# Kernel tuning notes

Hardware: AMD Instinct MI355X
Metric: run time of the kernel (lower is better)

## Reference

```python
import jax, jax.numpy as jnp
import numpy as np
from jax import lax


def setup_inputs() -> dict:
    key = jax.random.key(0)
    ks = jax.random.split(key, 9)
    B = 4096
    x = jax.random.normal(ks[0], (B, 1, 28, 28), jnp.float32)

    def init(k, shape, fan_in):
        return (jax.random.normal(k, shape, jnp.float32) / np.float32(np.sqrt(fan_in)))

    W1 = init(ks[1], (32, 1, 3, 3), 1 * 9)
    b1 = init(ks[2], (32,), 1 * 9)
    W2 = init(ks[3], (64, 32, 3, 3), 32 * 9)
    b2 = init(ks[4], (64,), 32 * 9)
    Wl1 = init(ks[5], (14 * 14 * 64, 128), 14 * 14 * 64)
    bl1 = init(ks[6], (128,), 14 * 14 * 64)
    Wl2 = init(ks[7], (128, 10), 128)
    bl2 = init(ks[8], (10,), 128)
    return {"x": x, "W1": W1, "b1": b1, "W2": W2, "b2": b2,
            "Wl1": Wl1, "bl1": bl1, "Wl2": Wl2, "bl2": bl2}


def _conv_same(h, W, b):
    # submanifold sparse conv == SAME-padded dense conv, output restricted to active sites
    y = lax.conv_general_dilated(h, W, window_strides=(1, 1), padding="SAME",
                                 dimension_numbers=("NCHW", "OIHW", "NCHW"))
    return y + b[None, :, None, None]


def reference(x, W1, b1, W2, b2, Wl1, bl1, Wl2, bl2):
    # active-site mask from Voxels.from_dense (nonzero pixels); submanifold convs keep it fixed
    mask = (jnp.abs(x) > 0).any(axis=1, keepdims=True).astype(x.dtype)  # [B,1,28,28]
    h = jax.nn.relu(_conv_same(x, W1, b1) * mask)   # [B,32,28,28]
    h = jax.nn.relu(_conv_same(h, W2, b2) * mask)   # [B,64,28,28]
    # sparse 2x2/2 max pool; inactive sites are 0 and post-ReLU actives are >=0,
    # so dense window max == sparse max, and all-inactive windows densify to 0
    B = h.shape[0]
    h = h.reshape(B, 64, 14, 2, 14, 2).max(axis=(3, 5))  # [B,64,14,14]
    h = h.reshape(B, 64 * 14 * 14)
    # dropout is identity in eval
    h = jax.nn.relu(h @ Wl1 + bl1)
    logits = h @ Wl2 + bl2
    return jax.nn.log_softmax(logits, axis=1)
```

## Files before the change

kernel.cpp:

```cpp
#include <hip/hip_runtime.h>
#include <math.h>

typedef __bf16 bf16;
typedef __bf16 bf16x8 __attribute__((ext_vector_type(8)));
typedef unsigned short u16;
typedef unsigned short u16x4 __attribute__((ext_vector_type(4)));
typedef unsigned short u16x8 __attribute__((ext_vector_type(8)));
typedef float f32x4 __attribute__((ext_vector_type(4)));
typedef float f32x16 __attribute__((ext_vector_type(16)));
typedef unsigned int u32x4 __attribute__((ext_vector_type(4)));

__global__ void prep_all(const float* __restrict__ W2, bf16* __restrict__ w2r,
                         const float* __restrict__ W1, bf16* __restrict__ w1f,
                         const float* __restrict__ Wl1, bf16* __restrict__ wl1t) {
    __shared__ float tile[32 * 129];
    const int b = blockIdx.x;
    const int t = threadIdx.x;
    if (b < 392) {
        const int s  = b >> 1;
        const int cg = b & 1;
        for (int e = t; e < 4096; e += 256) {
            int cl = e >> 7, n = e & 127;
            tile[cl * 129 + n] = Wl1[((long)(cg * 32 + cl) * 196 + s) * 128 + n];
        }
        __syncthreads();
        for (int e = t; e < 4096; e += 256) {
            int n = e >> 5, cl = e & 31;
            wl1t[(long)n * 12544 + s * 64 + cg * 32 + cl] = (bf16)tile[cl * 129 + n];
        }
    } else {
        int e = (b - 392) * 256 + t;
        if (e < 18432) {
            int j  = e & 7;
            int l  = (e >> 3) & 63;
            int f  = e >> 9;
            int s  = f >> 1;
            int nt = f & 1;
            int tap  = s >> 1;
            int ci   = (s & 1) * 16 + (l >> 5) * 8 + j;
            int cout = nt * 32 + (l & 31);
            w2r[e] = (bf16)W2[cout * 288 + ci * 9 + tap];
        } else {
            int e2 = e - 18432;
            if (e2 < 512) {
                int j = e2 & 7;
                int l = e2 >> 3;
                int k = (l >> 5) * 8 + j;
                int n = l & 31;
                w1f[e2] = (k < 9) ? (bf16)W1[n * 9 + k] : (bf16)0.f;
            }
        }
    }
}

__global__ __launch_bounds__(256, 3)
void conv_fused(const float* __restrict__ x, const float* __restrict__ b1,
                const bf16* __restrict__ w2r, const bf16* __restrict__ w1f,
                const float* __restrict__ b2, bf16* __restrict__ pooled)
{
    __shared__ __attribute__((aligned(16))) bf16  h1s[16 * 1032];
    __shared__ __attribute__((aligned(16))) bf16  Aim[512 * 16];
    __shared__ __attribute__((aligned(16))) u16   mrow[512];
    __shared__ __attribute__((aligned(16))) float mneg[98 * 4];
    __shared__ __attribute__((aligned(16))) bf16  xs[640];

    const int t    = threadIdx.x;
    const int lane = t & 63;
    const int wv   = t >> 6;
    const int img  = blockIdx.x >> 1;
    const int hb   = blockIdx.x & 1;
    const int nt   = wv & 1;
    const int wp   = wv >> 1;
    const int ml31 = lane & 31;
    const int lg   = lane >> 5;

    const float* xi = x + img * 784;

    bf16x8 breg[18];
    {
        const bf16x8* wp2 = (const bf16x8*)w2r;
        #pragma unroll
        for (int s = 0; s < 18; s++)
            breg[s] = wp2[(2 * s + nt) * 64 + lane];
    }
    const bf16x8 w1frag = *(const bf16x8*)&w1f[lane * 8];
    const float  b1r    = b1[ml31];
    const float  bias2  = b2[nt * 32 + ml31];

    for (int e = t; e < 640; e += 256) {
        int j  = e >> 5;
        int c  = e & 31;
        int xr = hb * 14 - 2 + j;
        int xc = c - 1;
        float v = 0.f;
        if (xr >= 0 && xr < 28 && xc >= 0 && xc < 28) v = xi[xr * 28 + xc];
        xs[e] = (bf16)v;
    }
    __syncthreads();

    const u16* xu = (const u16*)xs;
    #pragma unroll
    for (int pp = 0; pp < 2; pp++) {
        int p = t + pp * 256;
        int r = p >> 5, c = p & 31;
        int b = r * 32 + c - 1;
        u16 v0 = xu[b],      v1 = xu[b + 1],  v2 = xu[b + 2];
        u16 v3 = xu[b + 32], v4 = xu[b + 33], v5 = xu[b + 34];
        u16 v6 = xu[b + 64], v7 = xu[b + 65], v8 = xu[b + 66];
        u16x8 t0;
        t0[0] = v0; t0[1] = v1; t0[2] = v2; t0[3] = v3;
        t0[4] = v4; t0[5] = v5; t0[6] = v6; t0[7] = v7;
        u16x8 t1;
        #pragma unroll
        for (int j = 0; j < 8; j++) t1[j] = 0;
        t1[0] = v8;
        *(u16x8*)&Aim[p * 16]     = *(u16x8*)&t0;
        *(u16x8*)&Aim[p * 16 + 8] = *(u16x8*)&t1;
        mrow[p] = (c >= 1 && c <= 28 && (v4 & 0x7fff) != 0) ? 1 : 0;
    }
    for (int e = t; e < 392; e += 256) {
        int s   = e >> 2, q = e & 3;
        int spi = s / 14, spj = s - spi * 14;
        u16 cv = xu[(2 * spi + (q >> 1) + 2) * 32 + 2 * spj + (q & 1) + 1];
        mneg[e] = ((cv & 0x7fff) != 0) ? 0.f : -1e30f;
    }
    __syncthreads();

    for (int Mt = wv; Mt < 16; Mt += 4) {
        int m = Mt * 32 + ml31;
        bf16x8 af = *(const bf16x8*)&Aim[m * 16 + lg * 8];
        f32x16 acc;
        #pragma unroll
        for (int e = 0; e < 16; e++) acc[e] = b1r;
        acc = __builtin_amdgcn_mfma_f32_32x32x16_bf16(af, w1frag, acc, 0, 0, 0);
        const int rowb = Mt * 1032;
        #pragma unroll
        for (int run = 0; run < 4; run++) {
            int p0 = Mt * 32 + run * 8 + 4 * lg;
            u16x4 mk = *(const u16x4*)&mrow[p0];
            #pragma unroll
            for (int j = 0; j < 4; j++) {
                float s = acc[run * 4 + j];
                float o = (mk[j] != 0) ? fmaxf(s, 0.f) : 0.f;
                int col = run * 8 + 4 * lg + j;
                int swz = (col & 6) << 2;
                h1s[rowb + col * 32 + (ml31 ^ swz)] = (bf16)o;
            }
        }
    }
    __syncthreads();

    const int half = lg;
    const int cib  = half * 8;

    int q  = ml31 & 3;
    int pj = wp * 8 + (ml31 >> 2);
    int pi = 0;
    if (pj >= 14) { pj -= 14; pi = 1; }

    bf16* pout = pooled + (long)img * 12544 + hb * 98 * 64 + nt * 32 + ml31;

    for (int Mt = wp; Mt < 13; Mt += 2) {
        int row = 2 * pi + (q >> 1);
        if (row > 13) row = 13;
        int colb = 2 * pj + (q & 1);
        int rowb = row * 1032;

        int e0a[3], e1a[3];
        #pragma unroll
        for (int dc = 0; dc < 3; dc++) {
            int cc   = colb + dc;
            int swz  = (cc & 6) << 2;
            int base = rowb + cc * 32;
            e0a[dc] = base + (cib ^ swz);
            e1a[dc] = base + ((16 + cib) ^ swz);
        }

        f32x16 accA, accB = {};
        #pragma unroll
        for (int e = 0; e < 16; e++) accA[e] = bias2;

        #pragma unroll
        for (int dr = 0; dr < 3; dr++) {
            #pragma unroll
            for (int dc = 0; dc < 3; dc++) {
                const int tap = dr * 3 + dc;
                bf16x8 a0 = *(const bf16x8*)&h1s[e0a[dc] + dr * 1032];
                bf16x8 a1 = *(const bf16x8*)&h1s[e1a[dc] + dr * 1032];
                accA = __builtin_amdgcn_mfma_f32_32x32x16_bf16(a0, breg[2 * tap],     accA, 0, 0, 0);
                accB = __builtin_amdgcn_mfma_f32_32x32x16_bf16(a1, breg[2 * tap + 1], accB, 0, 0, 0);
            }
        }

        int slg = 8 * Mt + half;
        #pragma unroll
        for (int gg = 0; gg < 4; gg++) {
            if (slg < 98) {
                f32x4 mn = *(const f32x4*)&mneg[slg * 4];
                float v0 = accA[gg * 4 + 0] + accB[gg * 4 + 0] + mn[0];
                float v1 = accA[gg * 4 + 1] + accB[gg * 4 + 1] + mn[1];
                float v2 = accA[gg * 4 + 2] + accB[gg * 4 + 2] + mn[2];
                float v3 = accA[gg * 4 + 3] + accB[gg * 4 + 3] + mn[3];
                float pm = fmaxf(fmaxf(v0, v1), fmaxf(v2, v3));
                pout[slg * 64] = (bf16)fmaxf(pm, 0.f);
            }
            slg += 2;
        }

        pj += 2; if (pj >= 14) { pj -= 14; pi += 1; }
        pi += 1;
    }
}

__global__ __launch_bounds__(256, 4)
void fc1(const bf16* __restrict__ pooled, const bf16* __restrict__ wl1t,
         float* __restrict__ part)
{
    __shared__ __attribute__((aligned(16))) bf16 As[2][32 * 64];
    __shared__ __attribute__((aligned(16))) bf16 Bs[2][128 * 64];

    const int t    = threadIdx.x;
    const int lane = t & 63;
    const int wv   = t >> 6;
    const int ml   = lane & 15;
    const int kg   = lane >> 4;
    const int wm   = wv & 1;
    const int wn   = wv >> 1;
    const int m0   = blockIdx.x * 32;
    const int ks   = blockIdx.y;
    const int k0   = ks * 1792;

    const bf16* asrc;
    {
        int sub = t >> 7, i = t & 127;
        int r  = i >> 2;
        int jq = (i & 3) ^ ((r >> 1) & 3);
        asrc = pooled + (long)(m0 + r) * 12544 + k0 + sub * 32 + jq * 8;
    }
    const bf16* bsrc[4];
    #pragma unroll
    for (int u = 0; u < 4; u++) {
        int c  = u * 256 + t;
        int sub = c >> 9, i = c & 511;
        int r  = i >> 2;
        int jq = (i & 3) ^ ((r >> 1) & 3);
        bsrc[u] = wl1t + (long)r * 12544 + k0 + sub * 32 + jq * 8;
    }

    const int am = wm * 16 + ml;
    int aoff[2], boff[4];
    #pragma unroll
    for (int s = 0; s < 2; s++)
        aoff[s] = s * 1024 + ((am * 32 + kg * 8) ^ ((am & 6) << 2));
    #pragma unroll
    for (int j = 0; j < 4; j++) {
        int n = wn * 64 + j * 16 + ml;
        boff[j] = (n * 32 + kg * 8) ^ ((n & 6) << 2);
    }

    f32x4 acc[4];
    {
        f32x4 z = {0.f, 0.f, 0.f, 0.f};
        #pragma unroll
        for (int j = 0; j < 4; j++) acc[j] = z;
    }

    u32x4 ra = *(const u32x4*)asrc;
    u32x4 rb[4];
    #pragma unroll
    for (int u = 0; u < 4; u++) rb[u] = *(const u32x4*)bsrc[u];
    *(u32x4*)&As[0][t * 8] = ra;
    #pragma unroll
    for (int u = 0; u < 4; u++) *(u32x4*)&Bs[0][(u * 256 + t) * 8] = rb[u];

    for (int kt = 0; kt < 28; kt++) {
        __syncthreads();
        const int cur = kt & 1;
        if (kt < 27) {
            const int kb = (kt + 1) * 64;
            ra = *(const u32x4*)(asrc + kb);
            #pragma unroll
            for (int u = 0; u < 4; u++) rb[u] = *(const u32x4*)(bsrc[u] + kb);
        }
        #pragma unroll
        for (int s = 0; s < 2; s++) {
            bf16x8 af = *(const bf16x8*)&As[cur][aoff[s]];
            #pragma unroll
            for (int j = 0; j < 4; j++) {
                bf16x8 bf = *(const bf16x8*)&Bs[cur][s * 4096 + boff[j]];
                acc[j] = __builtin_amdgcn_mfma_f32_16x16x32_bf16(af, bf, acc[j], 0, 0, 0);
            }
        }
        if (kt < 27) {
            *(u32x4*)&As[cur ^ 1][t * 8] = ra;
            #pragma unroll
            for (int u = 0; u < 4; u++)
                *(u32x4*)&Bs[cur ^ 1][(u * 256 + t) * 8] = rb[u];
        }
    }

    float* pp = part + ((long)ks * 4096 + m0 + wm * 16) * 128 + wn * 64;
    #pragma unroll
    for (int j = 0; j < 4; j++)
        #pragma unroll
        for (int r = 0; r < 4; r++)
            pp[(kg * 4 + r) * 128 + j * 16 + ml] = acc[j][r];
}

__global__ __launch_bounds__(256)
void fc2_lsm(const float* __restrict__ part, const float* __restrict__ bl1,
             const float* __restrict__ Wl2, const float* __restrict__ bl2,
             float* __restrict__ out)
{
    const int wv   = threadIdx.x >> 6;
    const int lane = threadIdx.x & 63;
    const int img  = blockIdx.x * 4 + wv;
    const float* pb = part + (long)img * 128;

    float ac[10];
    #pragma unroll
    for (int c = 0; c < 10; c++) ac[c] = 0.f;

    #pragma unroll
    for (int u = 0; u < 2; u++) {
        int n = lane + 64 * u;
        float s = bl1[n];
        #pragma unroll
        for (int k = 0; k < 7; k++) s += pb[(long)k * 4096 * 128 + n];
        float h = s > 0.f ? s : 0.f;
        #pragma unroll
        for (int c = 0; c < 10; c++) ac[c] += h * Wl2[n * 10 + c];
    }
    #pragma unroll
    for (int o = 32; o > 0; o >>= 1)
        #pragma unroll
        for (int c = 0; c < 10; c++) ac[c] += __shfl_down(ac[c], o, 64);

    if (lane == 0) {
        float lg[10], mx = -1e30f;
        #pragma unroll
        for (int c = 0; c < 10; c++) {
            lg[c] = ac[c] + bl2[c];
            mx = lg[c] > mx ? lg[c] : mx;
        }
        float se = 0.f;
        #pragma unroll
        for (int c = 0; c < 10; c++) se += __expf(lg[c] - mx);
        float ls = __logf(se);
        #pragma unroll
        for (int c = 0; c < 10; c++) out[img * 10 + c] = lg[c] - mx - ls;
    }
}

extern "C" void kernel_launch(void* const* d_in, const int* in_sizes, int n_in,
                              void* d_out, int out_size, void* d_ws, size_t ws_size,
                              hipStream_t stream) {
    const float* x   = (const float*)d_in[0];
    const float* W1  = (const float*)d_in[1];
    const float* b1  = (const float*)d_in[2];
    const float* W2  = (const float*)d_in[3];
    const float* b2  = (const float*)d_in[4];
    const float* Wl1 = (const float*)d_in[5];
    const float* bl1 = (const float*)d_in[6];
    const float* Wl2 = (const float*)d_in[7];
    const float* bl2 = (const float*)d_in[8];
    float* out = (float*)d_out;

    char* ws = (char*)d_ws;
    bf16*  w2r    = (bf16*)ws;
    bf16*  w1f    = (bf16*)(ws + 40960);
    bf16*  wl1t   = (bf16*)(ws + 65536);
    bf16*  pooled = (bf16*)(ws + 65536 + 4194304);
    float* part   = (float*)(ws + 65536 + 4194304 + 102760448);

    prep_all  <<<466,            256, 0, stream>>>(W2, w2r, W1, w1f, Wl1, wl1t);
    conv_fused<<<8192,           256, 0, stream>>>(x, b1, w2r, w1f, b2, pooled);
    fc1       <<<dim3(128, 7),   256, 0, stream>>>(pooled, wl1t, part);
    fc2_lsm   <<<1024,           256, 0, stream>>>(part, bl1, Wl2, bl2, out);
}
```

Measured before the change: 269.2 us.

## Build conv1 im2col fragments in registers and merge conv2 accumulators

Conv1 no longer stages an im2col matrix and mask array in shared memory. Each wave now gathers its MFMA A-fragment directly from the padded input tile and computes the activity mask inline, which removes a pass, a barrier and about 17KB of LDS. Conv2 now chains both channel halves into a single accumulator instead of two independent ones, and both loops are marked unroll 1. These changes cut LDS use and registers, which may raise occupancy, but the single chained accumulator serialises back-to-back dependent MFMAs and can expose their latency.

```diff
diff --git a/kernel.cpp b/kernel.cpp
--- a/kernel.cpp
+++ b/kernel.cpp
@@ -59,8 +59,6 @@
                 const float* __restrict__ b2, bf16* __restrict__ pooled)
 {
     __shared__ __attribute__((aligned(16))) bf16  h1s[16 * 1032];
-    __shared__ __attribute__((aligned(16))) bf16  Aim[512 * 16];
-    __shared__ __attribute__((aligned(16))) u16   mrow[512];
     __shared__ __attribute__((aligned(16))) float mneg[98 * 4];
     __shared__ __attribute__((aligned(16))) bf16  xs[640];
 
@@ -99,50 +97,45 @@
     __syncthreads();
 
     const u16* xu = (const u16*)xs;
-    #pragma unroll
-    for (int pp = 0; pp < 2; pp++) {
-        int p = t + pp * 256;
-        int r = p >> 5, c = p & 31;
-        int b = r * 32 + c - 1;
-        u16 v0 = xu[b],      v1 = xu[b + 1],  v2 = xu[b + 2];
-        u16 v3 = xu[b + 32], v4 = xu[b + 33], v5 = xu[b + 34];
-        u16 v6 = xu[b + 64], v7 = xu[b + 65], v8 = xu[b + 66];
-        u16x8 t0;
-        t0[0] = v0; t0[1] = v1; t0[2] = v2; t0[3] = v3;
-        t0[4] = v4; t0[5] = v5; t0[6] = v6; t0[7] = v7;
-        u16x8 t1;
-        #pragma unroll
-        for (int j = 0; j < 8; j++) t1[j] = 0;
-        t1[0] = v8;
-        *(u16x8*)&Aim[p * 16]     = *(u16x8*)&t0;
-        *(u16x8*)&Aim[p * 16 + 8] = *(u16x8*)&t1;
-        mrow[p] = (c >= 1 && c <= 28 && (v4 & 0x7fff) != 0) ? 1 : 0;
-    }
+
     for (int e = t; e < 392; e += 256) {
         int s   = e >> 2, q = e & 3;
         int spi = s / 14, spj = s - spi * 14;
         u16 cv = xu[(2 * spi + (q >> 1) + 2) * 32 + 2 * spj + (q & 1) + 1];
         mneg[e] = ((cv & 0x7fff) != 0) ? 0.f : -1e30f;
     }
-    __syncthreads();
-
+
+    #pragma unroll 1
     for (int Mt = wv; Mt < 16; Mt += 4) {
-        int m = Mt * 32 + ml31;
-        bf16x8 af = *(const bf16x8*)&Aim[m * 16 + lg * 8];
+        const int bb = Mt * 32 + ml31 - 1;
+        u16x8 tv;
+        if (lg == 0) {
+            tv[0] = xu[bb];      tv[1] = xu[bb + 1];  tv[2] = xu[bb + 2];
+            tv[3] = xu[bb + 32]; tv[4] = xu[bb + 33]; tv[5] = xu[bb + 34];
+            tv[6] = xu[bb + 64]; tv[7] = xu[bb + 65];
+        } else {
+            #pragma unroll
+            for (int j = 0; j < 8; j++) tv[j] = 0;
+            tv[0] = xu[bb + 66];
+        }
+        bf16x8 af = *(bf16x8*)&tv;
+
         f32x16 acc;
         #pragma unroll
         for (int e = 0; e < 16; e++) acc[e] = b1r;
         acc = __builtin_amdgcn_mfma_f32_32x32x16_bf16(af, w1frag, acc, 0, 0, 0);
+
         const int rowb = Mt * 1032;
         #pragma unroll
         for (int run = 0; run < 4; run++) {
-            int p0 = Mt * 32 + run * 8 + 4 * lg;
-            u16x4 mk = *(const u16x4*)&mrow[p0];
+            const int cb = run * 8 + 4 * lg;
+            u16x4 ctr = *(const u16x4*)&xu[(Mt + 1) * 32 + cb];
             #pragma unroll
             for (int j = 0; j < 4; j++) {
+                int col = cb + j;
+                bool ok = (col >= 1) && (col <= 28) && ((ctr[j] & 0x7fff) != 0);
                 float s = acc[run * 4 + j];
-                float o = (mk[j] != 0) ? fmaxf(s, 0.f) : 0.f;
-                int col = run * 8 + 4 * lg + j;
+                float o = ok ? fmaxf(s, 0.f) : 0.f;
                 int swz = (col & 6) << 2;
                 h1s[rowb + col * 32 + (ml31 ^ swz)] = (bf16)o;
             }
@@ -150,8 +143,7 @@
     }
     __syncthreads();
 
-    const int half = lg;
-    const int cib  = half * 8;
+    const int cib = lg * 8;
 
     int q  = ml31 & 3;
     int pj = wp * 8 + (ml31 >> 2);
@@ -160,6 +152,7 @@
 
     bf16* pout = pooled + (long)img * 12544 + hb * 98 * 64 + nt * 32 + ml31;
 
+    #pragma unroll 1
     for (int Mt = wp; Mt < 13; Mt += 2) {
         int row = 2 * pi + (q >> 1);
         if (row > 13) row = 13;
@@ -176,9 +169,9 @@
             e1a[dc] = base + ((16 + cib) ^ swz);
         }
 
-        f32x16 accA, accB = {};
-        #pragma unroll
-        for (int e = 0; e < 16; e++) accA[e] = bias2;
+        f32x16 acc;
+        #pragma unroll
+        for (int e = 0; e < 16; e++) acc[e] = bias2;
 
         #pragma unroll
         for (int dr = 0; dr < 3; dr++) {
@@ -187,20 +180,20 @@
                 const int tap = dr * 3 + dc;
                 bf16x8 a0 = *(const bf16x8*)&h1s[e0a[dc] + dr * 1032];
                 bf16x8 a1 = *(const bf16x8*)&h1s[e1a[dc] + dr * 1032];
-                accA = __builtin_amdgcn_mfma_f32_32x32x16_bf16(a0, breg[2 * tap],     accA, 0, 0, 0);
-                accB = __builtin_amdgcn_mfma_f32_32x32x16_bf16(a1, breg[2 * tap + 1], accB, 0, 0, 0);
-            }
-        }
-
-        int slg = 8 * Mt + half;
+                acc = __builtin_amdgcn_mfma_f32_32x32x16_bf16(a0, breg[2 * tap],     acc, 0, 0, 0);
+                acc = __builtin_amdgcn_mfma_f32_32x32x16_bf16(a1, breg[2 * tap + 1], acc, 0, 0, 0);
+            }
+        }
+
+        int slg = 8 * Mt + lg;
         #pragma unroll
         for (int gg = 0; gg < 4; gg++) {
             if (slg < 98) {
                 f32x4 mn = *(const f32x4*)&mneg[slg * 4];
-                float v0 = accA[gg * 4 + 0] + accB[gg * 4 + 0] + mn[0];
-                float v1 = accA[gg * 4 + 1] + accB[gg * 4 + 1] + mn[1];
-                float v2 = accA[gg * 4 + 2] + accB[gg * 4 + 2] + mn[2];
-                float v3 = accA[gg * 4 + 3] + accB[gg * 4 + 3] + mn[3];
+                float v0 = acc[gg * 4 + 0] + mn[0];
+                float v1 = acc[gg * 4 + 1] + mn[1];
+                float v2 = acc[gg * 4 + 2] + mn[2];
+                float v3 = acc[gg * 4 + 3] + mn[3];
                 float pm = fmaxf(fmaxf(v0, v1), fmaxf(v2, v3));
                 pout[slg * 64] = (bf16)fmaxf(pm, 0.f);
             }
```

Measured after the change: 259.9 us. 3.4% less time.
